# Optimization experiments

Hardware: AMD Instinct MI355X
Metric: run time of the kernel (lower is better)

## Reference

```python
import jax, jax.numpy as jnp
import numpy as np
from jax import lax

B, D, S, H, W, T = 128, 512, 30, 14, 14, 12


def setup_inputs() -> dict:
    key = jax.random.key(0)
    ks = jax.random.split(key, 28)
    f = lambda k, shape: jax.random.normal(k, shape, jnp.float32) * 0.05
    return {
        "q": f(ks[0], (B, D)),
        "cws": f(ks[1], (B, D, S)),
        "KB": f(ks[2], (B, D, H, W)),
        "c0": f(ks[3], (B, D)),
        "m0": f(ks[4], (B, D)),
        "Wq": f(ks[5], (D, D)), "bq": f(ks[6], (D,)),
        "Wct": f(ks[7], (2 * D, D)), "bct": f(ks[8], (D,)),
        "wca": f(ks[9], (D,)), "bca": f(ks[10], ()),
        "Wm": f(ks[11], (D, D)), "bm": f(ks[12], (D,)),
        "Wkb": f(ks[13], (D, D)), "bkb": f(ks[14], (D,)),
        "Wrm": f(ks[15], (2 * D, D)), "brm": f(ks[16], (D,)),
        "wra": f(ks[17], (D,)), "bra": f(ks[18], ()),
        "Wwm": f(ks[19], (2 * D, D)), "bwm": f(ks[20], (D,)),
        "wwa": f(ks[21], (D,)), "bwa": f(ks[22], ()),
        "Wam": f(ks[23], (2 * D, D)), "bam": f(ks[24], (D,)),
        "Wg": f(ks[25], (D, D)), "bg": f(ks[26], (D,)),
        "steps": T,
    }


def _mac(q, cws, KB, c0, m0, Wq, bq, Wct, bct, wca, bca, Wm, bm, Wkb, bkb,
         Wrm, brm, wra, bra, Wwm, bwm, wwa, bwa, Wam, bam, Wg, bg, steps):
    b, d, h, w = KB.shape[0], KB.shape[1], KB.shape[2], KB.shape[3]
    KBp = jnp.transpose(KB, (0, 2, 3, 1))          # B,H,W,d
    KB2 = KBp @ Wkb + bkb                           # KB_transform (step-invariant)
    q_i = q @ Wq + bq                               # q_transform (step-invariant)

    nhist = steps + 1
    c_hist = jnp.zeros((nhist, b, d), KB.dtype).at[0].set(c0)
    m_hist = jnp.zeros((nhist, b, d), KB.dtype).at[0].set(m0)

    def step(carry, t):
        c_hist, m_hist, c_prev, m_prev = carry
        # ---- ControlUnit ----
        cq = jnp.concatenate([q_i, c_prev], axis=-1) @ Wct + bct   # B,d
        clog = jnp.einsum('bds,d->bs', cq[:, :, None] * cws, wca) + bca
        cattn = jax.nn.softmax(clog, axis=-1)                       # B,S
        c_i = jnp.einsum('bs,bds->bd', cattn, cws)
        # ---- ReadUnit ----
        mp = m_prev @ Wm + bm                                       # B,d
        I = mp[:, None, None, :] * KB2                              # B,H,W,d
        Im = jnp.concatenate([I, KBp], axis=-1) @ Wrm + brm         # B,H,W,d
        rlog = jnp.einsum('bhwd,d->bhw', c_i[:, None, None, :] * Im, wra) + bra
        rattn = jax.nn.softmax(rlog.reshape(b, -1), axis=-1).reshape(b, h, w)
        m_new = jnp.einsum('bhw,bhwd->bd', rattn, KBp)
        # ---- WriteUnit (self_attn + mem_gate) ----
        _m = jnp.concatenate([m_new, m_prev], axis=-1) @ Wwm + bwm
        slog = jnp.einsum('tbd,d->bt', c_i[None] * c_hist, wwa) + bwa
        valid = jnp.arange(nhist) <= t
        slog = jnp.where(valid[None, :], slog, jnp.float32(-1e9))
        sattn = jax.nn.softmax(slog, axis=-1)                       # B,T+1
        m_sa = jnp.einsum('bt,tbd->bd', sattn, m_hist)
        _m = jnp.concatenate([m_sa, _m], axis=-1) @ Wam + bam
        g = jax.nn.sigmoid(c_i @ Wg + bg)
        _m = g * m_prev + (1.0 - g) * _m
        c_hist = c_hist.at[t + 1].set(c_i)
        m_hist = m_hist.at[t + 1].set(_m)
        return (c_hist, m_hist, c_i, _m), None

    (c_hist, m_hist, c_last, m_last), _ = lax.scan(
        step, (c_hist, m_hist, c0, m0), jnp.arange(steps))
    return m_last


def reference(q, cws, KB, c0, m0, Wq, bq, Wct, bct, wca, bca, Wm, bm, Wkb, bkb,
              Wrm, brm, wra, bra, Wwm, bwm, wwa, bwa, Wam, bam, Wg, bg, steps):
    return _mac(q, cws, KB, c0, m0, Wq, bq, Wct, bct, wca, bca, Wm, bm, Wkb, bkb,
                Wrm, brm, wra, bra, Wwm, bwm, wwa, bwa, Wam, bam, Wg, bg, steps)
```

## Files before the change

### kernel.cpp

```cpp
#include <hip/hip_runtime.h>
#include <cstdint>

#define BB 128
#define DD 512
#define SS 30
#define PP 196
#define TT 12
#define BD (BB*DD)

typedef unsigned short ushortT;
typedef unsigned int uintT;

__device__ __forceinline__ float bf2f(ushortT u)
{
    return __uint_as_float(((uintT)u) << 16);
}
__device__ __forceinline__ ushortT f2bf(float f)
{
    uintT b = __float_as_uint(f);
    return (ushortT)((b + 0x7FFFu + ((b >> 16) & 1u)) >> 16);
}

struct GDesc {
    const float *A0, *A1;
    const float *W0, *W1;
    const float *bias;
    float *out;
    const float *e1;
    int nparts, epi, mblk, nblk, aux;
};
struct GPack { GDesc d[6]; };

__global__ __launch_bounds__(256)
void gemm4(GPack pk)
{
    GDesc d = pk.d[blockIdx.z];
    if ((int)blockIdx.x >= d.mblk || (int)blockIdx.y >= d.nblk) return;
    const int tid  = threadIdx.x;
    const int lane = tid & 63;
    const int wv   = __builtin_amdgcn_readfirstlane(tid >> 6);

    if (d.epi == 5) {
        int b = blockIdx.x * 2 + blockIdx.y;
        const float* sat = d.W0 + b * 16;
        float a0 = 0.f, a1 = 0.f;
        for (int tp = 0; tp <= d.aux; ++tp) {
            float s = sat[tp];
            const float* mh = d.A0 + (size_t)tp * BD + (size_t)b * DD;
            a0 = fmaf(s, mh[tid], a0);
            a1 = fmaf(s, mh[tid + 256], a1);
        }
        d.out[(size_t)b * DD + tid] = a0;
        d.out[(size_t)b * DD + tid + 256] = a1;
        return;
    }

    const int m0 = blockIdx.x * 2;
    const int c0 = blockIdx.y * 256;
    float acc0x = 0.f, acc0y = 0.f, acc0z = 0.f, acc0w = 0.f;
    float acc1x = 0.f, acc1y = 0.f, acc1z = 0.f, acc1w = 0.f;

    for (int p = 0; p < d.nparts; ++p) {
        const float* A = p ? d.A1 : d.A0;
        const float* W = p ? d.W1 : d.W0;
        const float* a = A + (size_t)m0 * 512 + wv * 128;
        const float4* Wb = (const float4*)(W + (size_t)(wv * 128) * 512 + c0) + lane;
        #pragma unroll 4
        for (int k = 0; k < 128; ++k) {
            float4 w4 = Wb[(size_t)k * 128];
            float a0 = a[k], a1 = a[512 + k];
            acc0x = fmaf(a0, w4.x, acc0x);  acc1x = fmaf(a1, w4.x, acc1x);
            acc0y = fmaf(a0, w4.y, acc0y);  acc1y = fmaf(a1, w4.y, acc1y);
            acc0z = fmaf(a0, w4.z, acc0z);  acc1z = fmaf(a1, w4.z, acc1z);
            acc0w = fmaf(a0, w4.w, acc0w);  acc1w = fmaf(a1, w4.w, acc1w);
        }
    }

    __shared__ float red[4][2][256];
    *(float4*)&red[wv][0][lane * 4] = make_float4(acc0x, acc0y, acc0z, acc0w);
    *(float4*)&red[wv][1][lane * 4] = make_float4(acc1x, acc1y, acc1z, acc1w);
    __syncthreads();

    for (int i = tid; i < 512; i += 256) {
        int mm = i >> 8, cl = i & 255;
        float s = (red[0][mm][cl] + red[1][mm][cl])
                + (red[2][mm][cl] + red[3][mm][cl]);
        int row = m0 + mm, col = c0 + cl;
        size_t o = (size_t)row * 512 + col;
        if (d.epi == 0)      d.out[o] = s + d.bias[col];
        else if (d.epi == 1) { float v = s + d.bias[col];
                               d.out[o] = 1.f / (1.f + __expf(-v)); }
        else if (d.epi == 4) d.out[o] = s + d.e1[o];
        else if (d.epi == 7) ((ushortT*)d.out)[o] = f2bf(s);
        else                 d.out[o] = s;
    }
}

struct SP {
    const float *cq, *cws, *wca, *bca, *wra, *wwa, *bwa;
    const ushortT *cwsTh;
    float *c_hist, *sattn, *vb;
    const float *msa, *mnw, *gb, *b2;
    const ushortT *WamH, *WAH, *WBH;
    float *m_hist, *dst;
    int t;
};

__global__ __launch_bounds__(512)
void stepA(SP P)
{
    const int tid = threadIdx.x;
    const int lane = tid & 63;
    __shared__ float cqw[512], ciw[512];
    __shared__ float clog2[32], cattn[32], slog[16];
    __shared__ float red[8][2][128];

    if ((int)blockIdx.x < 128) {
        if (P.t >= TT) return;
        int b = blockIdx.x, w = tid >> 6, t = P.t;
        cqw[tid] = P.cq[(size_t)b*DD + tid] * P.wca[tid];
        __syncthreads();
        for (int s = w; s < SS; s += 8) {
            const ushortT* row = P.cwsTh + ((size_t)b*SS + s)*DD;
            float a = 0.f;
            #pragma unroll
            for (int j = 0; j < 8; ++j)
                a = fmaf(cqw[lane + 64*j], bf2f(row[lane + 64*j]), a);
            for (int off = 32; off; off >>= 1) a += __shfl_xor(a, off, 64);
            if (lane == 0) clog2[s] = a;
        }
        __syncthreads();
        if (tid < 32) {
            float v = (tid < SS) ? clog2[tid] + P.bca[0] : -1e30f;
            float mx = v;
            for (int off = 16; off; off >>= 1) mx = fmaxf(mx, __shfl_xor(mx, off, 32));
            float e = (tid < SS) ? __expf(v - mx) : 0.f;
            float sm = e;
            for (int off = 16; off; off >>= 1) sm += __shfl_xor(sm, off, 32);
            cattn[tid] = e / sm;
        }
        __syncthreads();
        {
            const float* base = P.cws + (size_t)b*DD*SS + (size_t)tid*SS;
            float acc = 0.f;
            #pragma unroll
            for (int j = 0; j < SS; ++j) acc = fmaf(cattn[j], base[j], acc);
            P.c_hist[(size_t)(t+1)*BD + (size_t)b*DD + tid] = acc;
            P.vb[(size_t)b*DD + tid] = acc * P.wra[tid];
            ciw[tid] = acc * P.wwa[tid];
        }
        __syncthreads();
        for (int tp = tid >> 6; tp <= t; tp += 8) {
            const float* ch = P.c_hist + (size_t)tp*BD + (size_t)b*DD;
            float a = 0.f;
            #pragma unroll
            for (int j = 0; j < 8; ++j)
                a = fmaf(ciw[lane + 64*j], ch[lane + 64*j], a);
            for (int off = 32; off; off >>= 1) a += __shfl_xor(a, off, 64);
            if (lane == 0) slog[tp] = a;
        }
        __syncthreads();
        if (tid < 16) {
            float v = (tid <= t) ? slog[tid] + P.bwa[0] : -1e30f;
            float mx = v;
            for (int off = 8; off; off >>= 1) mx = fmaxf(mx, __shfl_xor(mx, off, 16));
            float e = (tid <= t) ? __expf(v - mx) : 0.f;
            float sm = e;
            for (int off = 8; off; off >>= 1) sm += __shfl_xor(sm, off, 16);
            P.sattn[b*16 + tid] = e / sm;
        }
    } else {
        if (P.t == 0) return;
        int gb_ = blockIdx.x - 128;
        int mt = gb_ >> 2, nc = gb_ & 3;
        int wv = __builtin_amdgcn_readfirstlane(tid >> 6);
        const int koff = wv * 64;
        const float* mprev = P.m_hist + (size_t)(P.t - 1) * BD;
        const int r0 = mt * 2;
        float ax0 = 0.f, ay0 = 0.f, ax1 = 0.f, ay1 = 0.f;

        const float* As[3] = { P.msa, P.mnw, mprev };
        const ushortT* Ws[3] = { P.WamH, P.WAH, P.WBH };
        #pragma unroll
        for (int seg = 0; seg < 3; ++seg) {
            const float* a = As[seg] + (size_t)r0 * 512 + koff;
            const uintT* Wb = (const uintT*)(Ws[seg] + (size_t)koff * 512 + nc * 128) + lane;
            #pragma unroll 8
            for (int k = 0; k < 64; ++k) {
                uintT w = Wb[(size_t)k * 256];
                float wx = __uint_as_float(w << 16);
                float wy = __uint_as_float(w & 0xFFFF0000u);
                float av0 = a[k], av1 = a[512 + k];
                ax0 = fmaf(av0, wx, ax0); ay0 = fmaf(av0, wy, ay0);
                ax1 = fmaf(av1, wx, ax1); ay1 = fmaf(av1, wy, ay1);
            }
        }
        *(float2*)&red[wv][0][lane*2] = make_float2(ax0, ay0);
        *(float2*)&red[wv][1][lane*2] = make_float2(ax1, ay1);
        __syncthreads();
        if (tid < 256) {
            int mm = tid >> 7, cl = tid & 127;
            float s = 0.f;
            #pragma unroll
            for (int j = 0; j < 8; ++j) s += red[j][mm][cl];
            int row = r0 + mm, col = nc*128 + cl;
            size_t o = (size_t)row*512 + col;
            float v = s + P.b2[col];
            float g = P.gb[o];
            float pv = mprev[o];
            P.dst[o] = g*pv + (1.f - g)*v;
        }
    }
}

__global__ __launch_bounds__(256)
void read1y(const ushortT* __restrict__ KBh, const float* __restrict__ ubuf,
            const float* __restrict__ mp, const float* __restrict__ WkbT,
            const float* __restrict__ vW, float* __restrict__ rlogp)
{
    int b = blockIdx.x, dg = blockIdx.y, tid = threadIdx.x;
    int lane = tid & 63, w = tid >> 6;
    __shared__ float red[4][64];
    __shared__ float yb[64];
    {
        const float* ur = ubuf + (size_t)b*512;
        const float* mr = mp + (size_t)b*512;
        const float* Wc = WkbT + dg*64 + lane;
        float s = 0.f;
        for (int k = w*128; k < w*128 + 128; ++k)
            s = fmaf(ur[k]*mr[k], Wc[(size_t)k*512], s);
        red[w][lane] = s;
    }
    __syncthreads();
    if (tid < 64)
        yb[tid] = (red[0][tid]+red[1][tid]) + (red[2][tid]+red[3][tid])
                + vW[(size_t)b*512 + dg*64 + tid];
    __syncthreads();
    float a0=0.f, a1=0.f, a2=0.f, a3=0.f;
    if (tid < PP) {
        const ushortT* kb = KBh + ((size_t)b*512 + dg*64)*PP + tid;
        #pragma unroll 4
        for (int dd = 0; dd < 64; dd += 4) {
            a0 = fmaf(bf2f(kb[(size_t)(dd+0)*PP]), yb[dd+0], a0);
            a1 = fmaf(bf2f(kb[(size_t)(dd+1)*PP]), yb[dd+1], a1);
            a2 = fmaf(bf2f(kb[(size_t)(dd+2)*PP]), yb[dd+2], a2);
            a3 = fmaf(bf2f(kb[(size_t)(dd+3)*PP]), yb[dd+3], a3);
        }
    }
    rlogp[((size_t)b*8 + dg)*256 + tid] = (a0+a1)+(a2+a3);
}

__global__ __launch_bounds__(256)
void read2(const ushortT* __restrict__ KBh, const float* __restrict__ rlogp,
           float* __restrict__ m_new)
{
    int b = blockIdx.x, dg = blockIdx.y;
    int tid = threadIdx.x, lane = tid & 63, w = tid >> 6;
    __shared__ float ex[256];
    __shared__ float wred[4];

    float v = -1e30f;
    if (tid < PP) {
        const float* rp = rlogp + (size_t)b*2048 + tid;
        float t0 = rp[0]    + rp[256];
        float t1 = rp[512]  + rp[768];
        float t2 = rp[1024] + rp[1280];
        float t3 = rp[1536] + rp[1792];
        v = (t0+t1)+(t2+t3);
    }
    float mx = v;
    for (int off = 32; off; off >>= 1) mx = fmaxf(mx, __shfl_xor(mx, off, 64));
    if (lane == 0) wred[w] = mx;
    __syncthreads();
    float gmax = fmaxf(fmaxf(wred[0], wred[1]), fmaxf(wred[2], wred[3]));
    float e = (tid < PP) ? __expf(v - gmax) : 0.f;
    float sm = e;
    for (int off = 32; off; off >>= 1) sm += __shfl_xor(sm, off, 64);
    __syncthreads();
    if (lane == 0) wred[w] = sm;
    __syncthreads();
    float inv = 1.f / ((wred[0]+wred[1]) + (wred[2]+wred[3]));
    ex[tid] = e * inv;
    __syncthreads();

    #pragma unroll 2
    for (int i = 0; i < 16; ++i) {
        int d = dg*64 + w*16 + i;
        const ushortT* row = KBh + ((size_t)b*512 + d)*PP;
        float a = ex[lane]       * bf2f(row[lane])
                + ex[lane + 64]  * bf2f(row[lane + 64])
                + ex[lane + 128] * bf2f(row[lane + 128]);
        if (lane < PP - 192) a = fmaf(ex[lane + 192], bf2f(row[lane + 192]), a);
        for (int off = 32; off; off >>= 1) a += __shfl_xor(a, off, 64);
        if (lane == 0) m_new[(size_t)b*512 + d] = a;
    }
}

struct SetupP {
    const float *Wrm, *Wkb, *cws, *KB, *c0v, *m0v, *bwm, *Wam, *Wam_bot, *bam;
    float *WrmTu, *WrmTv, *WkbT, *c_hist, *m_hist, *b2;
    ushortT *KBh, *cwsTh, *WamH;
};

__global__ __launch_bounds__(256)
void setup_misc(SetupP P)
{
    __shared__ float tile[32][33];
    int id = blockIdx.x, tid = threadIdx.x;

    if (id < 768) {
        int which = id >> 8, tj = id & 255;
        const float* src = (which == 0) ? P.Wrm
                         : (which == 1) ? (P.Wrm + 512*512) : P.Wkb;
        float* dst = (which == 0) ? P.WrmTu : (which == 1) ? P.WrmTv : P.WkbT;
        int bx = (tj & 15) * 32, by = (tj >> 4) * 32;
        int tx = tid & 31, ty = tid >> 5;
        #pragma unroll
        for (int i = 0; i < 32; i += 8)
            tile[ty+i][tx] = src[(size_t)(by+ty+i)*512 + bx+tx];
        __syncthreads();
        #pragma unroll
        for (int i = 0; i < 32; i += 8)
            dst[(size_t)(bx+ty+i)*512 + by+tx] = tile[tx][ty+i];
    } else if (id < 2816) {
        int j = id - 768;
        int b = j >> 4, dc = j & 15;
        const float* src = P.cws + ((size_t)b*DD + dc*32) * SS;
        for (int i = tid; i < 1024; i += 256) {
            int r = i >> 5, s = i & 31;
            if (s < SS) tile[r][s] = src[(size_t)r*SS + s];
        }
        __syncthreads();
        for (int i = tid; i < 1024; i += 256) {
            int s = i >> 5, r = i & 31;
            if (s < SS)
                P.cwsTh[((size_t)b*SS + s)*DD + dc*32 + r] = f2bf(tile[r][s]);
        }
    } else if (id < 9088) {
        size_t i = ((size_t)(id - 2816) * 256 + tid) * 8;
        #pragma unroll
        for (int j = 0; j < 8; ++j) {
            uintT bits = __float_as_uint(P.KB[i + j]);
            uintT r = (bits + 0x7FFFu + ((bits >> 16) & 1u)) >> 16;
            P.KBh[i + j] = (ushortT)r;
        }
    } else if (id < 9344) {
        int i = (id - 9088) * 256 + tid;
        P.c_hist[i] = P.c0v[i];
        P.m_hist[i] = P.m0v[i];
    } else if (id < 9352) {
        int lane = tid & 63, w = tid >> 6;
        int n = (id - 9344) * 64 + lane;
        float s = 0.f;
        for (int k = w*128; k < w*128 + 128; ++k)
            s = fmaf(P.bwm[k], P.Wam_bot[(size_t)k*512 + n], s);
        __shared__ float red[4][64];
        red[w][lane] = s;
        __syncthreads();
        if (tid < 64) {
            int nn = (id - 9344) * 64 + tid;
            P.b2[nn] = red[0][tid] + red[1][tid] + red[2][tid] + red[3][tid]
                     + P.bam[nn];
        }
    } else {
        size_t i = ((size_t)(id - 9352) * 256 + tid) * 8;
        #pragma unroll
        for (int j = 0; j < 8; ++j)
            P.WamH[i + j] = f2bf(P.Wam[i + j]);
    }
}

extern "C" void kernel_launch(void* const* d_in, const int* in_sizes, int n_in,
                              void* d_out, int out_size, void* d_ws, size_t ws_size,
                              hipStream_t stream)
{
    (void)in_sizes; (void)n_in; (void)out_size; (void)ws_size;
    const float* q   = (const float*)d_in[0];
    const float* cws = (const float*)d_in[1];
    const float* KB  = (const float*)d_in[2];
    const float* c0  = (const float*)d_in[3];
    const float* m0  = (const float*)d_in[4];
    const float* Wq  = (const float*)d_in[5];
    const float* bq  = (const float*)d_in[6];
    const float* Wct = (const float*)d_in[7];
    const float* bct = (const float*)d_in[8];
    const float* wca = (const float*)d_in[9];
    const float* bca = (const float*)d_in[10];
    const float* Wm  = (const float*)d_in[11];
    const float* bm  = (const float*)d_in[12];
    const float* Wkb = (const float*)d_in[13];
    const float* Wrm = (const float*)d_in[15];
    const float* wra = (const float*)d_in[17];
    const float* Wwm = (const float*)d_in[19];
    const float* bwm = (const float*)d_in[20];
    const float* wwa = (const float*)d_in[21];
    const float* bwa = (const float*)d_in[22];
    const float* Wam = (const float*)d_in[23];
    const float* bam = (const float*)d_in[24];
    const float* Wg  = (const float*)d_in[25];
    const float* bg  = (const float*)d_in[26];

    float* ws      = (float*)d_ws;
    float* c_hist  = ws;
    float* m_hist  = ws + 13*BD;
    float* qct     = ws + 26*BD;
    float* q_i     = ws + 27*BD;
    float* cq      = ws + 28*BD;
    float* mp      = ws + 29*BD;
    float* vb      = ws + 30*BD;
    float* ubuf    = ws + 31*BD;
    float* vW      = ws + 32*BD;
    float* gb      = ws + 33*BD;
    float* msa     = ws + 34*BD;
    float* mnw     = ws + 35*BD;
    float* sattn   = ws + 36*BD;
    float* rlogp   = ws + 37*BD;
    float* WrmTu   = ws + 41*BD;
    float* WrmTv   = ws + 45*BD;
    float* WkbT    = ws + 49*BD;
    float* b2      = ws + 61*BD;
    ushortT* cwsTh = (ushortT*)(ws + 62*BD);
    ushortT* KBh   = (ushortT*)(ws + 92*BD);
    ushortT* WamH  = (ushortT*)(ws + 190*BD);
    ushortT* WAH   = (ushortT*)(ws + 192*BD);
    ushortT* WBH   = (ushortT*)(ws + 194*BD);

    const float* Wct_bot = Wct + 512*512;
    const float* Wam_bot = Wam + 512*512;
    const float* Wwm_bot = Wwm + 512*512;
    dim3 blk(256);
    GDesc Z = { nullptr,nullptr,nullptr,nullptr,nullptr,nullptr,nullptr,
                1, 6, 0, 0, 0 };

    {
        SetupP S;
        S.Wrm = Wrm; S.Wkb = Wkb; S.cws = cws; S.KB = KB;
        S.c0v = c0; S.m0v = m0; S.bwm = bwm; S.Wam = Wam;
        S.Wam_bot = Wam_bot; S.bam = bam;
        S.WrmTu = WrmTu; S.WrmTv = WrmTv; S.WkbT = WkbT;
        S.c_hist = c_hist; S.m_hist = m_hist; S.b2 = b2;
        S.KBh = KBh; S.cwsTh = cwsTh; S.WamH = WamH;
        setup_misc<<<dim3(9480), blk, 0, stream>>>(S);
    }
    {
        GPack pk;
        pk.d[0] = { Wwm, nullptr, Wam_bot, nullptr, nullptr, (float*)WAH,
                    nullptr, 1, 7, 256, 2, 0 };
        pk.d[1] = { Wwm_bot, nullptr, Wam_bot, nullptr, nullptr, (float*)WBH,
                    nullptr, 1, 7, 256, 2, 0 };
        pk.d[2] = { q, nullptr, Wq, nullptr, bq, q_i, nullptr,
                    1, 0, 64, 2, 0 };
        pk.d[3] = Z; pk.d[4] = Z; pk.d[5] = Z;
        gemm4<<<dim3(256,2,3), blk, 0, stream>>>(pk);
    }
    {
        GPack pk;
        pk.d[0] = { q_i, nullptr, Wct, nullptr, bct, qct, nullptr,
                    1, 0, 64, 2, 0 };
        pk.d[1] = { q_i, c0, Wct, Wct_bot, bct, cq, nullptr,
                    2, 0, 64, 2, 0 };
        pk.d[2] = Z; pk.d[3] = Z; pk.d[4] = Z; pk.d[5] = Z;
        gemm4<<<dim3(64,2,2), blk, 0, stream>>>(pk);
    }

    for (int t = 0; t <= TT; ++t) {
        {
            SP P;
            P.cq = cq; P.cws = cws; P.cwsTh = cwsTh;
            P.wca = wca; P.bca = bca; P.wra = wra; P.wwa = wwa; P.bwa = bwa;
            P.c_hist = c_hist; P.sattn = sattn; P.vb = vb;
            P.msa = msa; P.mnw = mnw; P.gb = gb; P.b2 = b2;
            P.WamH = WamH; P.WAH = WAH; P.WBH = WBH;
            P.m_hist = m_hist;
            P.dst = (t == TT) ? (float*)d_out : (m_hist + (size_t)t * BD);
            P.t = t;
            stepA<<<dim3(384), dim3(512), 0, stream>>>(P);
        }
        if (t == TT) break;

        float* c_i = c_hist + (size_t)(t+1) * BD;
        {
            GPack pk;
            pk.d[0] = { vb, nullptr, WrmTu, nullptr, nullptr, ubuf, nullptr,
                        1, 6, 64, 2, 0 };
            pk.d[1] = { vb, nullptr, WrmTv, nullptr, nullptr, vW, nullptr,
                        1, 6, 64, 2, 0 };
            pk.d[2] = { c_i, nullptr, Wg, nullptr, bg, gb, nullptr,
                        1, 1, 64, 2, 0 };
            pk.d[3] = { c_i, nullptr, Wct_bot, nullptr, nullptr, cq, qct,
                        1, 4, 64, 2, 0 };
            pk.d[4] = { m_hist + (size_t)t * BD, nullptr, Wm, nullptr, bm, mp,
                        nullptr, 1, 0, 64, 2, 0 };
            pk.d[5] = { m_hist, nullptr, sattn, nullptr, nullptr, msa, nullptr,
                        1, 5, 64, 2, t };
            gemm4<<<dim3(64,2,6), blk, 0, stream>>>(pk);
        }
        read1y<<<dim3(BB,8), blk, 0, stream>>>(KBh, ubuf, mp, WkbT, vW, rlogp);
        read2<<<dim3(BB,8), blk, 0, stream>>>(KBh, rlogp, mnw);
    }
}
```

Baseline: 776.4 us.

## Store GEMM weights in bf16 and retile gemm4 to 8 rows by 128 columns

All weights fed to gemm4 are converted once to bf16 in the setup kernel, including the transposed Wrm halves, Wg, Wm, Wq, Wct and Wam_bot. gemm4 now reads packed bf16 pairs and computes 8 rows by 128 columns per block instead of 2 rows by 256, so each weight load is reused across more rows. This roughly halves weight bytes per launch and cuts redundant weight reads across blocks. The cost is reduced weight precision and fewer blocks per launch. The epi 5 path is reorganised to handle two batch rows per block, and sattn now comes in through e1.

```diff
diff --git a/kernel.cpp b/kernel.cpp
--- a/kernel.cpp
+++ b/kernel.cpp
@@ -23,7 +23,7 @@
 
 struct GDesc {
     const float *A0, *A1;
-    const float *W0, *W1;
+    const ushortT *W0, *W1;
     const float *bias;
     float *out;
     const float *e1;
@@ -41,48 +41,56 @@
     const int wv   = __builtin_amdgcn_readfirstlane(tid >> 6);
 
     if (d.epi == 5) {
-        int b = blockIdx.x * 2 + blockIdx.y;
-        const float* sat = d.W0 + b * 16;
-        float a0 = 0.f, a1 = 0.f;
-        for (int tp = 0; tp <= d.aux; ++tp) {
-            float s = sat[tp];
-            const float* mh = d.A0 + (size_t)tp * BD + (size_t)b * DD;
-            a0 = fmaf(s, mh[tid], a0);
-            a1 = fmaf(s, mh[tid + 256], a1);
-        }
-        d.out[(size_t)b * DD + tid] = a0;
-        d.out[(size_t)b * DD + tid + 256] = a1;
+        int bb = (blockIdx.x * 4 + blockIdx.y) * 2;
+        #pragma unroll
+        for (int b = bb; b < bb + 2; ++b) {
+            const float* sat = d.e1 + b * 16;
+            float a0 = 0.f, a1 = 0.f;
+            for (int tp = 0; tp <= d.aux; ++tp) {
+                float s = sat[tp];
+                const float* mh = d.A0 + (size_t)tp * BD + (size_t)b * DD;
+                a0 = fmaf(s, mh[tid], a0);
+                a1 = fmaf(s, mh[tid + 256], a1);
+            }
+            d.out[(size_t)b * DD + tid] = a0;
+            d.out[(size_t)b * DD + tid + 256] = a1;
+        }
         return;
     }
 
-    const int m0 = blockIdx.x * 2;
-    const int c0 = blockIdx.y * 256;
-    float acc0x = 0.f, acc0y = 0.f, acc0z = 0.f, acc0w = 0.f;
-    float acc1x = 0.f, acc1y = 0.f, acc1z = 0.f, acc1w = 0.f;
+    const int m0 = blockIdx.x * 8;
+    const int c0 = blockIdx.y * 128;
+    float accx[8], accy[8];
+    #pragma unroll
+    for (int m = 0; m < 8; ++m) { accx[m] = 0.f; accy[m] = 0.f; }
 
     for (int p = 0; p < d.nparts; ++p) {
         const float* A = p ? d.A1 : d.A0;
-        const float* W = p ? d.W1 : d.W0;
+        const ushortT* W = p ? d.W1 : d.W0;
         const float* a = A + (size_t)m0 * 512 + wv * 128;
-        const float4* Wb = (const float4*)(W + (size_t)(wv * 128) * 512 + c0) + lane;
+        const uintT* Wb = (const uintT*)(W + (size_t)(wv * 128) * 512 + c0) + lane;
         #pragma unroll 4
         for (int k = 0; k < 128; ++k) {
-            float4 w4 = Wb[(size_t)k * 128];
-            float a0 = a[k], a1 = a[512 + k];
-            acc0x = fmaf(a0, w4.x, acc0x);  acc1x = fmaf(a1, w4.x, acc1x);
-            acc0y = fmaf(a0, w4.y, acc0y);  acc1y = fmaf(a1, w4.y, acc1y);
-            acc0z = fmaf(a0, w4.z, acc0z);  acc1z = fmaf(a1, w4.z, acc1z);
-            acc0w = fmaf(a0, w4.w, acc0w);  acc1w = fmaf(a1, w4.w, acc1w);
-        }
-    }
-
-    __shared__ float red[4][2][256];
-    *(float4*)&red[wv][0][lane * 4] = make_float4(acc0x, acc0y, acc0z, acc0w);
-    *(float4*)&red[wv][1][lane * 4] = make_float4(acc1x, acc1y, acc1z, acc1w);
-    __syncthreads();
-
-    for (int i = tid; i < 512; i += 256) {
-        int mm = i >> 8, cl = i & 255;
+            uintT w = Wb[(size_t)k * 256];
+            float wx = __uint_as_float(w << 16);
+            float wy = __uint_as_float(w & 0xFFFF0000u);
+            #pragma unroll
+            for (int m = 0; m < 8; ++m) {
+                float av = a[m * 512 + k];
+                accx[m] = fmaf(av, wx, accx[m]);
+                accy[m] = fmaf(av, wy, accy[m]);
+            }
+        }
+    }
+
+    __shared__ float red[4][8][128];
+    #pragma unroll
+    for (int m = 0; m < 8; ++m)
+        *(float2*)&red[wv][m][lane * 2] = make_float2(accx[m], accy[m]);
+    __syncthreads();
+
+    for (int i = tid; i < 1024; i += 256) {
+        int mm = i >> 7, cl = i & 127;
         float s = (red[0][mm][cl] + red[1][mm][cl])
                 + (red[2][mm][cl] + red[3][mm][cl]);
         int row = m0 + mm, col = c0 + cl;
@@ -297,9 +305,11 @@
 }
 
 struct SetupP {
-    const float *Wrm, *Wkb, *cws, *KB, *c0v, *m0v, *bwm, *Wam, *Wam_bot, *bam;
-    float *WrmTu, *WrmTv, *WkbT, *c_hist, *m_hist, *b2;
-    ushortT *KBh, *cwsTh, *WamH;
+    const float *Wrm, *Wkb, *cws, *KB, *c0v, *m0v, *bwm;
+    const float *Wam, *Wam_bot, *bam, *Wg, *Wm, *Wq, *Wct;
+    float *WkbT, *c_hist, *m_hist, *b2;
+    ushortT *KBh, *cwsTh, *WamH, *WgH, *WmH, *WqH, *WambH, *WctHt, *WctHb;
+    ushortT *WrmTuH, *WrmTvH;
 };
 
 __global__ __launch_bounds__(256)
@@ -312,16 +322,22 @@
         int which = id >> 8, tj = id & 255;
         const float* src = (which == 0) ? P.Wrm
                          : (which == 1) ? (P.Wrm + 512*512) : P.Wkb;
-        float* dst = (which == 0) ? P.WrmTu : (which == 1) ? P.WrmTv : P.WkbT;
         int bx = (tj & 15) * 32, by = (tj >> 4) * 32;
         int tx = tid & 31, ty = tid >> 5;
         #pragma unroll
         for (int i = 0; i < 32; i += 8)
             tile[ty+i][tx] = src[(size_t)(by+ty+i)*512 + bx+tx];
         __syncthreads();
-        #pragma unroll
-        for (int i = 0; i < 32; i += 8)
-            dst[(size_t)(bx+ty+i)*512 + by+tx] = tile[tx][ty+i];
+        if (which == 2) {
+            #pragma unroll
+            for (int i = 0; i < 32; i += 8)
+                P.WkbT[(size_t)(bx+ty+i)*512 + by+tx] = tile[tx][ty+i];
+        } else {
+            ushortT* dst = which ? P.WrmTvH : P.WrmTuH;
+            #pragma unroll
+            for (int i = 0; i < 32; i += 8)
+                dst[(size_t)(bx+ty+i)*512 + by+tx] = f2bf(tile[tx][ty+i]);
+        }
     } else if (id < 2816) {
         int j = id - 768;
         int b = j >> 4, dc = j & 15;
@@ -339,11 +355,8 @@
     } else if (id < 9088) {
         size_t i = ((size_t)(id - 2816) * 256 + tid) * 8;
         #pragma unroll
-        for (int j = 0; j < 8; ++j) {
-            uintT bits = __float_as_uint(P.KB[i + j]);
-            uintT r = (bits + 0x7FFFu + ((bits >> 16) & 1u)) >> 16;
-            P.KBh[i + j] = (ushortT)r;
-        }
+        for (int j = 0; j < 8; ++j)
+            P.KBh[i + j] = f2bf(P.KB[i + j]);
     } else if (id < 9344) {
         int i = (id - 9088) * 256 + tid;
         P.c_hist[i] = P.c0v[i];
@@ -363,10 +376,24 @@
                      + P.bam[nn];
         }
     } else {
-        size_t i = ((size_t)(id - 9352) * 256 + tid) * 8;
+        int j = id - 9352;
+        int which = j >> 7, blk = j & 127;
+        const float* src = (which == 0) ? P.Wam
+                         : (which == 1) ? P.Wg
+                         : (which == 2) ? P.Wm
+                         : (which == 3) ? P.Wq
+                         : (which == 4) ? P.Wam_bot
+                         : (which == 5) ? P.Wct : (P.Wct + 512*512);
+        ushortT* dst = (which == 0) ? P.WamH
+                     : (which == 1) ? P.WgH
+                     : (which == 2) ? P.WmH
+                     : (which == 3) ? P.WqH
+                     : (which == 4) ? P.WambH
+                     : (which == 5) ? P.WctHt : P.WctHb;
+        size_t i = ((size_t)blk * 256 + tid) * 8;
         #pragma unroll
-        for (int j = 0; j < 8; ++j)
-            P.WamH[i + j] = f2bf(P.Wam[i + j]);
+        for (int jj = 0; jj < 8; ++jj)
+            dst[i + jj] = f2bf(src[i + jj]);
     }
 }
 
@@ -415,8 +442,6 @@
     float* mnw     = ws + 35*BD;
     float* sattn   = ws + 36*BD;
     float* rlogp   = ws + 37*BD;
-    float* WrmTu   = ws + 41*BD;
-    float* WrmTv   = ws + 45*BD;
     float* WkbT    = ws + 49*BD;
     float* b2      = ws + 61*BD;
     ushortT* cwsTh = (ushortT*)(ws + 62*BD);
@@ -424,8 +449,15 @@
     ushortT* WamH  = (ushortT*)(ws + 190*BD);
     ushortT* WAH   = (ushortT*)(ws + 192*BD);
     ushortT* WBH   = (ushortT*)(ws + 194*BD);
-
-    const float* Wct_bot = Wct + 512*512;
+    ushortT* WgH   = (ushortT*)(ws + 196*BD);
+    ushortT* WmH   = (ushortT*)(ws + 198*BD);
+    ushortT* WqH   = (ushortT*)(ws + 200*BD);
+    ushortT* WambH = (ushortT*)(ws + 202*BD);
+    ushortT* WctHt = (ushortT*)(ws + 204*BD);
+    ushortT* WctHb = (ushortT*)(ws + 206*BD);
+    ushortT* WrmTuH= (ushortT*)(ws + 208*BD);
+    ushortT* WrmTvH= (ushortT*)(ws + 210*BD);
+
     const float* Wam_bot = Wam + 512*512;
     const float* Wwm_bot = Wwm + 512*512;
     dim3 blk(256);
@@ -435,32 +467,35 @@
     {
         SetupP S;
         S.Wrm = Wrm; S.Wkb = Wkb; S.cws = cws; S.KB = KB;
-        S.c0v = c0; S.m0v = m0; S.bwm = bwm; S.Wam = Wam;
-        S.Wam_bot = Wam_bot; S.bam = bam;
-        S.WrmTu = WrmTu; S.WrmTv = WrmTv; S.WkbT = WkbT;
-        S.c_hist = c_hist; S.m_hist = m_hist; S.b2 = b2;
-        S.KBh = KBh; S.cwsTh = cwsTh; S.WamH = WamH;
-        setup_misc<<<dim3(9480), blk, 0, stream>>>(S);
+        S.c0v = c0; S.m0v = m0; S.bwm = bwm;
+        S.Wam = Wam; S.Wam_bot = Wam_bot; S.bam = bam;
+        S.Wg = Wg; S.Wm = Wm; S.Wq = Wq; S.Wct = Wct;
+        S.WkbT = WkbT; S.c_hist = c_hist; S.m_hist = m_hist; S.b2 = b2;
+        S.KBh = KBh; S.cwsTh = cwsTh;
+        S.WamH = WamH; S.WgH = WgH; S.WmH = WmH; S.WqH = WqH;
+        S.WambH = WambH; S.WctHt = WctHt; S.WctHb = WctHb;
+        S.WrmTuH = WrmTuH; S.WrmTvH = WrmTvH;
+        setup_misc<<<dim3(10248), blk, 0, stream>>>(S);
     }
     {
         GPack pk;
-        pk.d[0] = { Wwm, nullptr, Wam_bot, nullptr, nullptr, (float*)WAH,
-                    nullptr, 1, 7, 256, 2, 0 };
-        pk.d[1] = { Wwm_bot, nullptr, Wam_bot, nullptr, nullptr, (float*)WBH,
-                    nullptr, 1, 7, 256, 2, 0 };
-        pk.d[2] = { q, nullptr, Wq, nullptr, bq, q_i, nullptr,
-                    1, 0, 64, 2, 0 };
+        pk.d[0] = { Wwm, nullptr, WambH, nullptr, nullptr, (float*)WAH,
+                    nullptr, 1, 7, 64, 4, 0 };
+        pk.d[1] = { Wwm_bot, nullptr, WambH, nullptr, nullptr, (float*)WBH,
+                    nullptr, 1, 7, 64, 4, 0 };
+        pk.d[2] = { q, nullptr, WqH, nullptr, bq, q_i, nullptr,
+                    1, 0, 16, 4, 0 };
         pk.d[3] = Z; pk.d[4] = Z; pk.d[5] = Z;
-        gemm4<<<dim3(256,2,3), blk, 0, stream>>>(pk);
+        gemm4<<<dim3(64,4,3), blk, 0, stream>>>(pk);
     }
     {
         GPack pk;
-        pk.d[0] = { q_i, nullptr, Wct, nullptr, bct, qct, nullptr,
-                    1, 0, 64, 2, 0 };
-        pk.d[1] = { q_i, c0, Wct, Wct_bot, bct, cq, nullptr,
-                    2, 0, 64, 2, 0 };
+        pk.d[0] = { q_i, nullptr, WctHt, nullptr, bct, qct, nullptr,
+                    1, 0, 16, 4, 0 };
+        pk.d[1] = { q_i, c0, WctHt, WctHb, bct, cq, nullptr,
+                    2, 0, 16, 4, 0 };
         pk.d[2] = Z; pk.d[3] = Z; pk.d[4] = Z; pk.d[5] = Z;
-        gemm4<<<dim3(64,2,2), blk, 0, stream>>>(pk);
+        gemm4<<<dim3(16,4,2), blk, 0, stream>>>(pk);
     }
 
     for (int t = 0; t <= TT; ++t) {
@@ -481,19 +516,19 @@
         float* c_i = c_hist + (size_t)(t+1) * BD;
         {
             GPack pk;
-            pk.d[0] = { vb, nullptr, WrmTu, nullptr, nullptr, ubuf, nullptr,
-                        1, 6, 64, 2, 0 };
-            pk.d[1] = { vb, nullptr, WrmTv, nullptr, nullptr, vW, nullptr,
-                        1, 6, 64, 2, 0 };
-            pk.d[2] = { c_i, nullptr, Wg, nullptr, bg, gb, nullptr,
-                        1, 1, 64, 2, 0 };
-            pk.d[3] = { c_i, nullptr, Wct_bot, nullptr, nullptr, cq, qct,
-                        1, 4, 64, 2, 0 };
-            pk.d[4] = { m_hist + (size_t)t * BD, nullptr, Wm, nullptr, bm, mp,
-                        nullptr, 1, 0, 64, 2, 0 };
-            pk.d[5] = { m_hist, nullptr, sattn, nullptr, nullptr, msa, nullptr,
-                        1, 5, 64, 2, t };
-            gemm4<<<dim3(64,2,6), blk, 0, stream>>>(pk);
+            pk.d[0] = { vb, nullptr, WrmTuH, nullptr, nullptr, ubuf, nullptr,
+                        1, 6, 16, 4, 0 };
+            pk.d[1] = { vb, nullptr, WrmTvH, nullptr, nullptr, vW, nullptr,
+                        1, 6, 16, 4, 0 };
+            pk.d[2] = { c_i, nullptr, WgH, nullptr, bg, gb, nullptr,
+                        1, 1, 16, 4, 0 };
+            pk.d[3] = { c_i, nullptr, WctHb, nullptr, nullptr, cq, qct,
+                        1, 4, 16, 4, 0 };
+            pk.d[4] = { m_hist + (size_t)t * BD, nullptr, WmH, nullptr, bm, mp,
+                        nullptr, 1, 0, 16, 4, 0 };
+            pk.d[5] = { m_hist, nullptr, nullptr, nullptr, nullptr, msa, sattn,
+                        1, 5, 16, 4, t };
+            gemm4<<<dim3(16,4,6), blk, 0, stream>>>(pk);
         }
         read1y<<<dim3(BB,8), blk, 0, stream>>>(KBh, ubuf, mp, WkbT, vW, rlogp);
         read2<<<dim3(BB,8), blk, 0, stream>>>(KBh, rlogp, mnw);
```

Result: faster. 756.3 us (-2.6%).
